# Performance work log

Measured on AMD Instinct MI355X. Metric: run time of the kernel, lower is better.

The kernel has to match this reference:

```python
import jax, jax.numpy as jnp
import numpy as np

B, S, D, H, DFF = 2, 2048, 1024, 16, 4096
DH = D // H
EPS = 1e-12


def _layer_norm(x, g, b):
    mu = jnp.mean(x, axis=-1, keepdims=True)
    var = jnp.mean(jnp.square(x - mu), axis=-1, keepdims=True)
    return (x - mu) * jax.lax.rsqrt(var + EPS) * g + b


def setup_inputs() -> dict:
    key = jax.random.key(0)
    ks = jax.random.split(key, 12)
    s = 0.02
    return {
        "query": jax.random.normal(ks[0], (B, S, D), jnp.float32),
        "key_in": jax.random.normal(ks[1], (B, S, D), jnp.float32),
        "value_in": jax.random.normal(ks[2], (B, S, D), jnp.float32),
        "attention_mask": jnp.zeros((B, 1, 1, S), jnp.float32),
        # weights stored [in, out] (i.e., torch Linear weight transposed)
        "Wq": jax.random.normal(ks[3], (D, D), jnp.float32) * s,
        "bq": jnp.zeros((D,), jnp.float32),
        "Wk": jax.random.normal(ks[4], (D, D), jnp.float32) * s,
        "bk": jnp.zeros((D,), jnp.float32),
        "Wv": jax.random.normal(ks[5], (D, D), jnp.float32) * s,
        "bv": jnp.zeros((D,), jnp.float32),
        "Wo": jax.random.normal(ks[6], (D, D), jnp.float32) * s,
        "bo": jnp.zeros((D,), jnp.float32),
        "ln1_g": jnp.ones((D,), jnp.float32),
        "ln1_b": jnp.zeros((D,), jnp.float32),
        "Wi": jax.random.normal(ks[7], (D, DFF), jnp.float32) * s,
        "bi": jnp.zeros((DFF,), jnp.float32),
        "Wd": jax.random.normal(ks[8], (DFF, D), jnp.float32) * s,
        "bd": jnp.zeros((D,), jnp.float32),
        "ln2_g": jnp.ones((D,), jnp.float32),
        "ln2_b": jnp.zeros((D,), jnp.float32),
    }


def reference(query, key_in, value_in, attention_mask, Wq, bq, Wk, bk, Wv, bv,
              Wo, bo, ln1_g, ln1_b, Wi, bi, Wd, bd, ln2_g, ln2_b):
    # projections -> [B, H, S, DH]
    q = (query @ Wq + bq).reshape(B, S, H, DH).transpose(0, 2, 1, 3)
    k = (key_in @ Wk + bk).reshape(B, S, H, DH).transpose(0, 2, 1, 3)
    v = (value_in @ Wv + bv).reshape(B, S, H, DH).transpose(0, 2, 1, 3)
    # eager attention: full [B,H,S,S] score matrix, as in the source
    scores = jnp.einsum("bhqd,bhkd->bhqk", q, k) / jnp.sqrt(jnp.float32(DH))
    scores = scores + attention_mask
    probs = jax.nn.softmax(scores, axis=-1)  # dropout p=0 -> identity
    ctx = jnp.einsum("bhqk,bhkd->bhqd", probs, v)
    ctx = ctx.transpose(0, 2, 1, 3).reshape(B, S, D)
    attn_out = ctx @ Wo + bo
    attn_out = _layer_norm(attn_out + query, ln1_g, ln1_b)
    inter = jax.nn.gelu(attn_out @ Wi + bi, approximate=False)
    layer_out = inter @ Wd + bd
    return _layer_norm(layer_out + attn_out, ln2_g, ln2_b)
```

## Files before the change

### kernel.cpp

```cpp
#include <hip/hip_runtime.h>
#include <hip/hip_bf16.h>
#include <cmath>

#define B_   2
#define S_   2048
#define D_   1024
#define H_   16
#define DFF_ 4096
#define DH_  64
#define M_   (B_*S_)

typedef __bf16 bfx8 __attribute__((ext_vector_type(8)));
typedef __bf16 bfx4 __attribute__((ext_vector_type(4)));
typedef float  fx4  __attribute__((ext_vector_type(4)));

__device__ __forceinline__ float fast_exp2(float x) {
  float r;
  asm volatile("v_exp_f32 %0, %1" : "=v"(r) : "v"(x));
  return r;
}

__device__ __forceinline__ float fast_erf(float x) {
  float ax = fabsf(x);
  float t  = __builtin_amdgcn_rcpf(fmaf(0.3275911f, ax, 1.0f));
  float p  = fmaf(1.061405429f, t, -1.453152027f);
  p = fmaf(p, t, 1.421413741f);
  p = fmaf(p, t, -0.284496736f);
  p = fmaf(p, t, 0.254829592f);
  p = p * t;
  float e  = fast_exp2(-ax * ax * 1.44269504f);
  float r  = 1.0f - p * e;
  return copysignf(r, x);
}

__device__ __forceinline__ void gload_lds16(const void* g, void* l) {
  __builtin_amdgcn_global_load_lds((__attribute__((address_space(1))) void*)(g),
                                   (__attribute__((address_space(3))) void*)(l),
                                   16, 0, 0);
}

struct CvtArgs { const float* in[3]; __bf16* out[3]; };

__global__ __launch_bounds__(256)
void to_bf16_3_kernel(CvtArgs args, int n) {
  int z = blockIdx.y;
  int i = (blockIdx.x * 256 + threadIdx.x) * 4;
  if (i < n) {
    float4 v = *(const float4*)(args.in[z] + i);
    bfx4 o;
    o[0] = (__bf16)v.x; o[1] = (__bf16)v.y; o[2] = (__bf16)v.z; o[3] = (__bf16)v.w;
    *(bfx4*)(args.out[z] + i) = o;
  }
}

__global__ __launch_bounds__(256)
void scale_mask_kernel(const float* __restrict__ in, float* __restrict__ out, int n) {
  int i = blockIdx.x * 256 + threadIdx.x;
  if (i < n) out[i] = in[i] * 1.44269504f;
}

__global__ __launch_bounds__(256)
void transpose_conv_kernel(const float* __restrict__ in, __bf16* __restrict__ out,
                           int R, int C) {
  __shared__ float t[32][33];
  int r0 = blockIdx.y * 32, c0 = blockIdx.x * 32;
  int tx = threadIdx.x, ty = threadIdx.y;
#pragma unroll
  for (int j = 0; j < 4; ++j) {
    int r = ty + j * 8;
    t[r][tx] = in[(size_t)(r0 + r) * C + c0 + tx];
  }
  __syncthreads();
#pragma unroll
  for (int j = 0; j < 4; ++j) {
    int c = ty + j * 8;
    out[(size_t)(c0 + c) * R + r0 + tx] = (__bf16)t[tx][c];
  }
}

__global__ __launch_bounds__(256)
void transpose_v_kernel(const __bf16* __restrict__ vb, __bf16* __restrict__ vt) {
  __shared__ __bf16 t[32][33];
  int bh = blockIdx.z;
  int b = bh >> 4, h = bh & 15;
  int s0 = blockIdx.x * 32, d0 = blockIdx.y * 32;
  int tx = threadIdx.x, ty = threadIdx.y;
#pragma unroll
  for (int j = 0; j < 4; ++j) {
    int s = ty + j * 8;
    t[s][tx] = vb[(size_t)((b * S_ + s0 + s) * H_ + h) * DH_ + d0 + tx];
  }
  __syncthreads();
#pragma unroll
  for (int j = 0; j < 4; ++j) {
    int d = ty + j * 8;
    vt[(size_t)(bh * DH_ + d0 + d) * S_ + s0 + tx] = t[tx][d];
  }
}

template<int MODE, int TBN>
__device__ __forceinline__ void gemm_body(const __bf16* __restrict__ A,
                                          const __bf16* __restrict__ Bt,
                                          const float* __restrict__ bias,
                                          const void* __restrict__ res,
                                          void* __restrict__ out,
                                          int Ndim, int Kdim,
                                          int m0, int n0,
                                          __bf16* As, __bf16* Bs) {
  const int tid  = threadIdx.x;
  const int lane = tid & 63;
  const int w    = tid >> 6;
  const int wm   = w >> 1, wn = w & 1;
  constexpr int NF = TBN / 32;

  fx4 acc[4][NF];
#pragma unroll
  for (int i = 0; i < 4; ++i)
#pragma unroll
    for (int j = 0; j < NF; ++j) acc[i][j] = {0.f, 0.f, 0.f, 0.f};

  const int KT = Kdim / 64;
  for (int kt = 0; kt < KT; ++kt) {
    __syncthreads();
    const int kb0 = kt * 64;
#pragma unroll
    for (int i = 0; i < 4; ++i) {
      int o   = tid * 16 + i * 4096;
      int row = o >> 7, cb = o & 127;
      int cbs = cb ^ ((row & 7) << 4);
      gload_lds16((const char*)A + ((size_t)(m0 + row) * Kdim + kb0) * 2 + cbs,
                  (char*)As + o);
    }
#pragma unroll
    for (int i = 0; i < TBN / 32; ++i) {
      int o   = tid * 16 + i * 4096;
      int row = o >> 7, cb = o & 127;
      int cbs = cb ^ ((row & 7) << 4);
      gload_lds16((const char*)Bt + ((size_t)(n0 + row) * Kdim + kb0) * 2 + cbs,
                  (char*)Bs + o);
    }
    __syncthreads();

#pragma unroll
    for (int kk = 0; kk < 2; ++kk) {
      bfx8 afr[4], bfr[NF];
      const int cb = kk * 64 + ((lane >> 4) << 4);
#pragma unroll
      for (int mf = 0; mf < 4; ++mf) {
        int row = wm * 64 + mf * 16 + (lane & 15);
        afr[mf] = *(const bfx8*)((const char*)As + row * 128 + (cb ^ ((row & 7) << 4)));
      }
#pragma unroll
      for (int nf = 0; nf < NF; ++nf) {
        int row = wn * (TBN / 2) + nf * 16 + (lane & 15);
        bfr[nf] = *(const bfx8*)((const char*)Bs + row * 128 + (cb ^ ((row & 7) << 4)));
      }
#pragma unroll
      for (int mf = 0; mf < 4; ++mf)
#pragma unroll
        for (int nf = 0; nf < NF; ++nf)
          acc[mf][nf] = __builtin_amdgcn_mfma_f32_16x16x32_bf16(afr[mf], bfr[nf],
                                                                acc[mf][nf], 0, 0, 0);
    }
  }

#pragma unroll
  for (int mf = 0; mf < 4; ++mf) {
#pragma unroll
    for (int nf = 0; nf < NF; ++nf) {
      int col = n0 + wn * (TBN / 2) + nf * 16 + (lane & 15);
      float bvl = bias[col];
#pragma unroll
      for (int r = 0; r < 4; ++r) {
        int rowg = m0 + wm * 64 + mf * 16 + ((lane >> 4) << 2) + r;
        float v = acc[mf][nf][r] + bvl;
        if (MODE == 2) v = 0.5f * v * (1.0f + fast_erf(v * 0.70710678118654752f));
        if (MODE == 4) v += (float)((const __bf16*)res)[(size_t)rowg * Ndim + col];
        if (MODE == 1) ((float*)out)[(size_t)rowg * Ndim + col] = v;
        else           ((__bf16*)out)[(size_t)rowg * Ndim + col] = (__bf16)v;
      }
    }
  }
}

template<int MODE, int TBN>
__global__ __launch_bounds__(256)
void gemm_kernel(const __bf16* __restrict__ A, const __bf16* __restrict__ Bt,
                 const float* __restrict__ bias, const void* __restrict__ res,
                 void* __restrict__ out, int Ndim, int Kdim) {
  __shared__ alignas(16) __bf16 As[128 * 64];
  __shared__ alignas(16) __bf16 Bs[TBN * 64];
  gemm_body<MODE, TBN>(A, Bt, bias, res, out, Ndim, Kdim,
                       blockIdx.y * 128, blockIdx.x * TBN, As, Bs);
}

__device__ __forceinline__ void stage_a256(const __bf16* __restrict__ A, int m0,
                                           int Kdim, int tile, int h, char* Asm) {
  char* dst = Asm + (tile & 1) * 32768;
  const int kb0 = tile * 64;
  const int tid = threadIdx.x;
#pragma unroll
  for (int it = 0; it < 2; ++it) {
    int o = tid * 16 + it * 8192;
    int lrow = o >> 7, cb = o & 127;
    int r = (lrow & 63) + h * 64 + ((lrow >> 6) << 7);
    int csrc = cb ^ ((r & 7) << 4);
    gload_lds16((const char*)A + ((size_t)(m0 + r) * Kdim + kb0) * 2 + csrc,
                dst + r * 128 + cb);
  }
}
__device__ __forceinline__ void stage_b256(const __bf16* __restrict__ Bt, int n0,
                                           int Kdim, int tile, int h, char* Bsm) {
  char* dst = Bsm + (tile & 1) * 32768;
  const int kb0 = tile * 64;
  const int tid = threadIdx.x;
#pragma unroll
  for (int it = 0; it < 2; ++it) {
    int o = tid * 16 + it * 8192;
    int lrow = o >> 7, cb = o & 127;
    int r = h * 128 + lrow;
    int csrc = cb ^ ((r & 7) << 4);
    gload_lds16((const char*)Bt + ((size_t)(n0 + r) * Kdim + kb0) * 2 + csrc,
                dst + r * 128 + cb);
  }
}

template<int MODE>
__device__ __forceinline__ void gemm256_body(const __bf16* __restrict__ A,
                                             const __bf16* __restrict__ Bt,
                                             const float* __restrict__ bias,
                                             void* __restrict__ out,
                                             int Ndim, int Kdim, int m0, int n0) {
  extern __shared__ char smem[];
  char* Asm = smem;
  char* Bsm = smem + 65536;
  const int tid  = threadIdx.x;
  const int lane = tid & 63;
  const int w    = tid >> 6;
  const int wm   = w >> 2;
  const int wn   = w & 3;
  const int g    = lane >> 4;
  const int ql   = lane & 15;
  const int KT   = Kdim / 64;

  fx4 acc[8][4];
#pragma unroll
  for (int i = 0; i < 8; ++i)
#pragma unroll
    for (int j = 0; j < 4; ++j) acc[i][j] = {0.f, 0.f, 0.f, 0.f};

  stage_a256(A, m0, Kdim, 0, 0, Asm);
  stage_a256(A, m0, Kdim, 0, 1, Asm);
  stage_b256(Bt, n0, Kdim, 0, 0, Bsm);
  stage_b256(Bt, n0, Kdim, 0, 1, Bsm);
  stage_a256(A, m0, Kdim, 1, 0, Asm);
  asm volatile("s_waitcnt vmcnt(2)" ::: "memory");
  __builtin_amdgcn_s_barrier();
  __builtin_amdgcn_sched_barrier(0);

  for (int t = 0; t < KT; ++t) {
    const char* Ab = Asm + (t & 1) * 32768;
    const char* Bb = Bsm + (t & 1) * 32768;
#pragma unroll
    for (int p = 0; p < 4; ++p) {
      const int ah = p >> 1, kk = p & 1;
      if (p == 0 && t + 1 < KT) stage_a256(A, m0, Kdim, t + 1, 1, Asm);
      if (p == 1 && t + 1 < KT) stage_b256(Bt, n0, Kdim, t + 1, 0, Bsm);
      if (p == 2 && t + 1 < KT) stage_b256(Bt, n0, Kdim, t + 1, 1, Bsm);
      if (p == 3 && t + 2 < KT) stage_a256(A, m0, Kdim, t + 2, 0, Asm);
      __builtin_amdgcn_sched_barrier(0);

      bfx8 af[4], bf[4];
      const int cbv = kk * 64 + g * 16;
#pragma unroll
      for (int j = 0; j < 4; ++j) {
        int arow = wm * 128 + (ah * 4 + j) * 16 + ql;
        af[j] = *(const bfx8*)(Ab + arow * 128 + (cbv ^ ((arow & 7) << 4)));
      }
#pragma unroll
      for (int nf = 0; nf < 4; ++nf) {
        int brow = wn * 64 + nf * 16 + ql;
        bf[nf] = *(const bfx8*)(Bb + brow * 128 + (cbv ^ ((brow & 7) << 4)));
      }
      __builtin_amdgcn_sched_barrier(0);
      __builtin_amdgcn_s_barrier();
      asm volatile("s_waitcnt lgkmcnt(0)" ::: "memory");
      __builtin_amdgcn_sched_barrier(0);
      __builtin_amdgcn_s_setprio(1);
#pragma unroll
      for (int j = 0; j < 4; ++j)
#pragma unroll
        for (int nf = 0; nf < 4; ++nf)
          acc[ah * 4 + j][nf] = __builtin_amdgcn_mfma_f32_16x16x32_bf16(
              af[j], bf[nf], acc[ah * 4 + j][nf], 0, 0, 0);
      __builtin_amdgcn_s_setprio(0);
      __builtin_amdgcn_s_barrier();
      __builtin_amdgcn_sched_barrier(0);
    }
    if (t + 1 < KT) {
      if (t + 2 < KT) asm volatile("s_waitcnt vmcnt(2)" ::: "memory");
      else            asm volatile("s_waitcnt vmcnt(0)" ::: "memory");
      __builtin_amdgcn_s_barrier();
      __builtin_amdgcn_sched_barrier(0);
    }
  }

#pragma unroll
  for (int mf = 0; mf < 8; ++mf) {
#pragma unroll
    for (int nf = 0; nf < 4; ++nf) {
      int col = n0 + wn * 64 + nf * 16 + ql;
      float bvl = bias[col];
#pragma unroll
      for (int r = 0; r < 4; ++r) {
        int rowg = m0 + wm * 128 + mf * 16 + g * 4 + r;
        float v = acc[mf][nf][r] + bvl;
        if (MODE == 2) v = 0.5f * v * (1.0f + fast_erf(v * 0.70710678118654752f));
        if (MODE == 1) ((float*)out)[(size_t)rowg * Ndim + col] = v;
        else          ((__bf16*)out)[(size_t)rowg * Ndim + col] = (__bf16)v;
      }
    }
  }
}

template<int MODE>
__global__ __launch_bounds__(512)
void gemm256_kernel(const __bf16* __restrict__ A, const __bf16* __restrict__ Bt,
                    const float* __restrict__ bias, void* __restrict__ out,
                    int Ndim, int Kdim) {
  gemm256_body<MODE>(A, Bt, bias, out, Ndim, Kdim,
                     blockIdx.y * 256, blockIdx.x * 256);
}

struct QKVArgs {
  const __bf16* A[3]; const __bf16* Bt[3]; const float* bias[3]; __bf16* out[3];
};

__global__ __launch_bounds__(512)
void qkv256_kernel(QKVArgs args, int Ndim, int Kdim) {
  int z = blockIdx.z;
  gemm256_body<0>(args.A[z], args.Bt[z], args.bias[z], (void*)args.out[z],
                  Ndim, Kdim, blockIdx.y * 256, blockIdx.x * 256);
}

__global__ __launch_bounds__(512)
void attn_kernel(const __bf16* __restrict__ Qb, const __bf16* __restrict__ Kb,
                 const __bf16* __restrict__ Vt, const float* __restrict__ mask2,
                 __bf16* __restrict__ ctx) {
  __shared__ alignas(16) __bf16 Ks[3 * 64 * 64];
  __shared__ alignas(16) __bf16 Vs[3 * 64 * 64];
  __shared__ alignas(16) __bf16 Ps[8 * 16 * 64];
  __shared__ alignas(16) float  Ms[2048];

  const int tid  = threadIdx.x;
  const int lane = tid & 63;
  const int w    = tid >> 6;
  const int g    = lane >> 4;
  const int ql   = lane & 15;
  const int bh   = blockIdx.y;
  const int b    = bh >> 4;
  const int h    = bh & 15;
  const int q0   = blockIdx.x * 128;

  const size_t kbase  = ((size_t)(b * S_)) * D_ + h * DH_;
  const size_t vtbase = (size_t)bh * DH_ * S_;
  const int NT = S_ / 64;

  char* Qsm = (char*)Ps;
  const size_t qbase = ((size_t)(b * S_) + q0) * D_ + h * DH_;
#pragma unroll
  for (int i = 0; i < 2; ++i) {
    int o   = tid * 16 + i * 8192;
    int row = o >> 7, cb = o & 127;
    int cbs = cb ^ ((row & 7) << 4);
    gload_lds16((const char*)Qb + (qbase + (size_t)row * D_) * 2 + cbs, Qsm + o);
  }
  {
    int o = tid * 16;
    gload_lds16((const char*)mask2 + (size_t)b * S_ * 4 + o, (char*)Ms + o);
  }
  {
    int o   = tid * 16;
    int row = o >> 7, cb = o & 127;
    int cbs = cb ^ ((row & 7) << 4);
    gload_lds16((const char*)Kb + (kbase + (size_t)row * D_) * 2 + cbs, (char*)Ks + o);
    gload_lds16((const char*)Vt + (vtbase + (size_t)row * S_) * 2 + cbs, (char*)Vs + o);
    gload_lds16((const char*)Kb + (kbase + (size_t)(64 + row) * D_) * 2 + cbs,
                (char*)Ks + 8192 + o);
    gload_lds16((const char*)Vt + (vtbase + (size_t)row * S_ + 64) * 2 + cbs,
                (char*)Vs + 8192 + o);
  }
  asm volatile("s_waitcnt vmcnt(4)" ::: "memory");
  __builtin_amdgcn_s_barrier();
  __builtin_amdgcn_sched_barrier(0);

  bfx8 aq[2];
  {
    int row = w * 16 + ql;
#pragma unroll
    for (int kk = 0; kk < 2; ++kk) {
      int cb = kk * 64 + g * 16;
      aq[kk] = *(const bfx8*)(Qsm + row * 128 + (cb ^ ((row & 7) << 4)));
    }
  }
  __syncthreads();
  asm volatile("s_waitcnt vmcnt(2)" ::: "memory");
  __builtin_amdgcn_s_barrier();
  __builtin_amdgcn_sched_barrier(0);

  float mrun = -1e30f, lrun = 0.f;
  fx4 acc[4];
#pragma unroll
  for (int d = 0; d < 4; ++d) acc[d] = {0.f, 0.f, 0.f, 0.f};

  char* pw = (char*)Ps + w * 2048;
  const float SCL = 0.18033688f;

  for (int t = 0; t < NT; ++t) {
    const int kv0 = t * 64;
    if (t + 2 < NT) {
      int o   = tid * 16;
      int row = o >> 7, cb = o & 127;
      int cbs = cb ^ ((row & 7) << 4);
      int nkv = kv0 + 128;
      int bo  = ((t + 2) % 3) * 8192;
      gload_lds16((const char*)Kb + (kbase + (size_t)(nkv + row) * D_) * 2 + cbs,
                  (char*)Ks + bo + o);
      gload_lds16((const char*)Vt + (vtbase + (size_t)row * S_ + nkv) * 2 + cbs,
                  (char*)Vs + bo + o);
    }
    __builtin_amdgcn_sched_barrier(0);
    if (t > 0) {
      if (t + 2 < NT)      asm volatile("s_waitcnt vmcnt(4)" ::: "memory");
      else if (t + 1 < NT) asm volatile("s_waitcnt vmcnt(2)" ::: "memory");
      else                 asm volatile("s_waitcnt vmcnt(0)" ::: "memory");
      __builtin_amdgcn_s_barrier();
      __builtin_amdgcn_sched_barrier(0);
    }
    const char* Kc = (const char*)Ks + (t % 3) * 8192;
    const char* Vc = (const char*)Vs + (t % 3) * 8192;

    fx4 sc[4];
#pragma unroll
    for (int nf = 0; nf < 4; ++nf) sc[nf] = {0.f, 0.f, 0.f, 0.f};
#pragma unroll
    for (int kk = 0; kk < 2; ++kk) {
      const int cb = kk * 64 + g * 16;
      bfx8 bk[4];
#pragma unroll
      for (int nf = 0; nf < 4; ++nf) {
        int row = nf * 16 + ql;
        bk[nf] = *(const bfx8*)(Kc + row * 128 + (cb ^ ((row & 7) << 4)));
      }
#pragma unroll
      for (int nf = 0; nf < 4; ++nf)
        sc[nf] = __builtin_amdgcn_mfma_f32_16x16x32_bf16(bk[nf], aq[kk], sc[nf], 0, 0, 0);
    }

    float sv[4][4];
#pragma unroll
    for (int nf = 0; nf < 4; ++nf) {
      float4 mk = *(const float4*)((const char*)Ms + (kv0 + nf * 16 + g * 4) * 4);
      sv[nf][0] = sc[nf][0] * SCL + mk.x;
      sv[nf][1] = sc[nf][1] * SCL + mk.y;
      sv[nf][2] = sc[nf][2] * SCL + mk.z;
      sv[nf][3] = sc[nf][3] * SCL + mk.w;
    }
    float t0 = fmaxf(fmaxf(sv[0][0], sv[0][1]), fmaxf(sv[0][2], sv[0][3]));
    float t1 = fmaxf(fmaxf(sv[1][0], sv[1][1]), fmaxf(sv[1][2], sv[1][3]));
    float t2 = fmaxf(fmaxf(sv[2][0], sv[2][1]), fmaxf(sv[2][2], sv[2][3]));
    float t3 = fmaxf(fmaxf(sv[3][0], sv[3][1]), fmaxf(sv[3][2], sv[3][3]));
    float mx = fmaxf(fmaxf(t0, t1), fmaxf(t2, t3));
    mx = fmaxf(mx, __shfl_xor(mx, 16));
    mx = fmaxf(mx, __shfl_xor(mx, 32));

    if (!__all(mx <= mrun + 8.0f)) {
      float mnew  = fmaxf(mrun, mx);
      float alpha = fast_exp2(mrun - mnew);
      lrun *= alpha;
      float af[4];
#pragma unroll
      for (int r = 0; r < 4; ++r) af[r] = __shfl(alpha, g * 4 + r);
#pragma unroll
      for (int d = 0; d < 4; ++d)
#pragma unroll
        for (int r = 0; r < 4; ++r) acc[d][r] *= af[r];
      mrun = mnew;
    }

    float ps[4];
#pragma unroll
    for (int nf = 0; nf < 4; ++nf) {
#pragma unroll
      for (int r = 0; r < 4; ++r) sv[nf][r] = fast_exp2(sv[nf][r] - mrun);
      ps[nf] = (sv[nf][0] + sv[nf][1]) + (sv[nf][2] + sv[nf][3]);
    }
    float rs = (ps[0] + ps[1]) + (ps[2] + ps[3]);
    rs += __shfl_xor(rs, 16);
    rs += __shfl_xor(rs, 32);
    lrun += rs;

#pragma unroll
    for (int nf = 0; nf < 4; ++nf) {
      bfx4 pv;
      pv[0] = (__bf16)sv[nf][0]; pv[1] = (__bf16)sv[nf][1];
      pv[2] = (__bf16)sv[nf][2]; pv[3] = (__bf16)sv[nf][3];
      int c = (nf * 32 + g * 8) ^ ((ql & 7) << 4);
      *(bfx4*)(pw + ql * 128 + c) = pv;
    }

    asm volatile("s_waitcnt lgkmcnt(0)" ::: "memory");
    __builtin_amdgcn_sched_barrier(0);

#pragma unroll
    for (int kk = 0; kk < 2; ++kk) {
      int prow = ql;
      int cb   = kk * 64 + g * 16;
      bfx8 ap  = *(const bfx8*)((const char*)pw + prow * 128 + (cb ^ ((prow & 7) << 4)));
#pragma unroll
      for (int d = 0; d < 4; ++d) {
        int vrow = d * 16 + ql;
        bfx8 bv  = *(const bfx8*)(Vc + vrow * 128 + (cb ^ ((vrow & 7) << 4)));
        acc[d] = __builtin_amdgcn_mfma_f32_16x16x32_bf16(ap, bv, acc[d], 0, 0, 0);
      }
    }

    __builtin_amdgcn_s_barrier();
    __builtin_amdgcn_sched_barrier(0);
  }

  float linv = 1.0f / lrun;
#pragma unroll
  for (int r = 0; r < 4; ++r) {
    float inv = __shfl(linv, g * 4 + r);
    int qrow = q0 + w * 16 + g * 4 + r;
    size_t base = ((size_t)(b * S_) + qrow) * D_ + h * DH_;
#pragma unroll
    for (int d = 0; d < 4; ++d)
      ctx[base + d * 16 + ql] = (__bf16)(acc[d][r] * inv);
  }
}

template<bool WRITE_BF16>
__global__ __launch_bounds__(256)
void ln_kernel(const __bf16* __restrict__ a,
               const float* __restrict__ g, const float* __restrict__ beta,
               float* __restrict__ outf, __bf16* __restrict__ outb) {
  const int row = blockIdx.x;
  const int tid = threadIdx.x;
  const size_t base = (size_t)row * D_;
  bfx4 xa = *(const bfx4*)(a + base + tid * 4);
  float x[4] = {(float)xa[0], (float)xa[1], (float)xa[2], (float)xa[3]};
  float s = x[0] + x[1] + x[2] + x[3];
#pragma unroll
  for (int m = 1; m < 64; m <<= 1) s += __shfl_xor(s, m);
  __shared__ float red[8];
  if ((tid & 63) == 0) red[tid >> 6] = s;
  __syncthreads();
  float mu = (red[0] + red[1] + red[2] + red[3]) * (1.0f / D_);
  float v0 = 0.f;
#pragma unroll
  for (int i = 0; i < 4; ++i) { float d = x[i] - mu; v0 += d * d; }
#pragma unroll
  for (int m = 1; m < 64; m <<= 1) v0 += __shfl_xor(v0, m);
  if ((tid & 63) == 0) red[4 + (tid >> 6)] = v0;
  __syncthreads();
  float var = (red[4] + red[5] + red[6] + red[7]) * (1.0f / D_);
  float rs = rsqrtf(var + 1e-12f);
#pragma unroll
  for (int i = 0; i < 4; ++i) {
    int col = tid * 4 + i;
    x[i] = (x[i] - mu) * rs * g[col] + beta[col];
  }
  if (WRITE_BF16) {
    bfx4 o;
    o[0] = (__bf16)x[0]; o[1] = (__bf16)x[1]; o[2] = (__bf16)x[2]; o[3] = (__bf16)x[3];
    *(bfx4*)(outb + base + tid * 4) = o;
  } else {
    *(float4*)(outf + base + tid * 4) = make_float4(x[0], x[1], x[2], x[3]);
  }
}

extern "C" void kernel_launch(void* const* d_in, const int* in_sizes, int n_in,
                              void* d_out, int out_size, void* d_ws, size_t ws_size,
                              hipStream_t stream) {
  const float* query    = (const float*)d_in[0];
  const float* key_in   = (const float*)d_in[1];
  const float* value_in = (const float*)d_in[2];
  const float* mask     = (const float*)d_in[3];
  const float* Wq = (const float*)d_in[4];  const float* bq = (const float*)d_in[5];
  const float* Wk = (const float*)d_in[6];  const float* bk = (const float*)d_in[7];
  const float* Wv = (const float*)d_in[8];  const float* bv = (const float*)d_in[9];
  const float* Wo = (const float*)d_in[10]; const float* bo = (const float*)d_in[11];
  const float* ln1g = (const float*)d_in[12]; const float* ln1b = (const float*)d_in[13];
  const float* Wi = (const float*)d_in[14]; const float* bi = (const float*)d_in[15];
  const float* Wd = (const float*)d_in[16]; const float* bd = (const float*)d_in[17];
  const float* ln2g = (const float*)d_in[18]; const float* ln2b = (const float*)d_in[19];

  char* ws = (char*)d_ws;
  const size_t MB = 1ull << 20;
  if (ws_size < 112 * MB) return;

  __bf16* xq   = (__bf16*)(ws + 0 * MB);
  __bf16* xk   = (__bf16*)(ws + 8 * MB);
  float*  mask2= (float*)(ws + 8 * MB);
  __bf16* xv   = (__bf16*)(ws + 16 * MB);
  __bf16* x1b  = (__bf16*)(ws + 16 * MB);
  __bf16* qb   = (__bf16*)(ws + 24 * MB);
  __bf16* inter= (__bf16*)(ws + 24 * MB);
  __bf16* kb   = (__bf16*)(ws + 32 * MB);
  __bf16* vb   = (__bf16*)(ws + 40 * MB);
  __bf16* alinb= (__bf16*)(ws + 40 * MB);
  __bf16* vt   = (__bf16*)(ws + 48 * MB);
  __bf16* ctxb = (__bf16*)(ws + 56 * MB);
  __bf16* ffb  = (__bf16*)(ws + 56 * MB);
  __bf16* wqt  = (__bf16*)(ws + 88 * MB);
  __bf16* wkt  = (__bf16*)(ws + 90 * MB);
  __bf16* wvt  = (__bf16*)(ws + 92 * MB);
  __bf16* wot  = (__bf16*)(ws + 94 * MB);
  __bf16* wit  = (__bf16*)(ws + 96 * MB);
  __bf16* wdt  = (__bf16*)(ws + 104 * MB);

  dim3 b256(256);
  dim3 tblk(32, 8);
  const int n1 = M_ * D_;

  CvtArgs ca;
  ca.in[0] = query; ca.in[1] = key_in; ca.in[2] = value_in;
  ca.out[0] = xq;   ca.out[1] = xk;    ca.out[2] = xv;
  to_bf16_3_kernel<<<dim3(n1 / 1024, 3), b256, 0, stream>>>(ca, n1);

  transpose_conv_kernel<<<dim3(D_ / 32, D_ / 32), tblk, 0, stream>>>(Wq, wqt, D_, D_);
  transpose_conv_kernel<<<dim3(D_ / 32, D_ / 32), tblk, 0, stream>>>(Wk, wkt, D_, D_);
  transpose_conv_kernel<<<dim3(D_ / 32, D_ / 32), tblk, 0, stream>>>(Wv, wvt, D_, D_);
  transpose_conv_kernel<<<dim3(D_ / 32, D_ / 32), tblk, 0, stream>>>(Wo, wot, D_, D_);
  transpose_conv_kernel<<<dim3(DFF_ / 32, D_ / 32), tblk, 0, stream>>>(Wi, wit, D_, DFF_);
  transpose_conv_kernel<<<dim3(D_ / 32, DFF_ / 32), tblk, 0, stream>>>(Wd, wdt, DFF_, D_);

  QKVArgs qa;
  qa.A[0] = xq;  qa.A[1] = xk;  qa.A[2] = xv;
  qa.Bt[0] = wqt; qa.Bt[1] = wkt; qa.Bt[2] = wvt;
  qa.bias[0] = bq; qa.bias[1] = bk; qa.bias[2] = bv;
  qa.out[0] = qb; qa.out[1] = kb; qa.out[2] = vb;
  qkv256_kernel<<<dim3(D_ / 256, M_ / 256, 3), dim3(512), 131072, stream>>>(qa, D_, D_);

  transpose_v_kernel<<<dim3(S_ / 32, 2, B_ * H_), tblk, 0, stream>>>(vb, vt);

  scale_mask_kernel<<<dim3((B_ * S_ + 255) / 256), b256, 0, stream>>>(mask, mask2, B_ * S_);

  attn_kernel<<<dim3(S_ / 128, B_ * H_), dim3(512), 0, stream>>>(qb, kb, vt, mask2, ctxb);

  gemm_kernel<4, 64><<<dim3(D_ / 64, M_ / 128), b256, 0, stream>>>(ctxb, wot, bo, xq, (void*)alinb, D_, D_);

  ln_kernel<true><<<dim3(M_), b256, 0, stream>>>(alinb, ln1g, ln1b, nullptr, x1b);

  gemm256_kernel<2><<<dim3(DFF_ / 256, M_ / 256), dim3(512), 131072, stream>>>(x1b, wit, bi, (void*)inter, DFF_, D_);

  gemm_kernel<4, 64><<<dim3(D_ / 64, M_ / 128), b256, 0, stream>>>(inter, wdt, bd, x1b, (void*)ffb, D_, DFF_);

  ln_kernel<false><<<dim3(M_), b256, 0, stream>>>(ffb, ln2g, ln2b, (float*)d_out, nullptr);
}
```

Before: 269.4 us.

## Double-buffer LDS in generic GEMM and batch weight transposes into one launch

```diff
diff --git a/kernel.cpp b/kernel.cpp
--- a/kernel.cpp
+++ b/kernel.cpp
@@ -59,12 +59,27 @@
   if (i < n) out[i] = in[i] * 1.44269504f;
 }
 
+struct TrArgs { const float* in[6]; __bf16* out[6]; };
+
 __global__ __launch_bounds__(256)
-void transpose_conv_kernel(const float* __restrict__ in, __bf16* __restrict__ out,
-                           int R, int C) {
+void transpose_all_kernel(TrArgs a) {
   __shared__ float t[32][33];
-  int r0 = blockIdx.y * 32, c0 = blockIdx.x * 32;
-  int tx = threadIdx.x, ty = threadIdx.y;
+  int bid = blockIdx.x;
+  int wsel, tr, tc, R, C;
+  if (bid < 4096) {
+    wsel = bid >> 10; int l = bid & 1023;
+    tr = l >> 5; tc = l & 31; R = D_; C = D_;
+  } else if (bid < 8192) {
+    wsel = 4; int l = bid - 4096;
+    tr = l >> 7; tc = l & 127; R = D_; C = DFF_;
+  } else {
+    wsel = 5; int l = bid - 8192;
+    tr = l >> 5; tc = l & 31; R = DFF_; C = D_;
+  }
+  const float* in = a.in[wsel];
+  __bf16* out = a.out[wsel];
+  int r0 = tr * 32, c0 = tc * 32;
+  int tx = threadIdx.x & 31, ty = threadIdx.x >> 5;
 #pragma unroll
   for (int j = 0; j < 4; ++j) {
     int r = ty + j * 8;
@@ -99,19 +114,18 @@
 }
 
 template<int MODE, int TBN>
-__device__ __forceinline__ void gemm_body(const __bf16* __restrict__ A,
-                                          const __bf16* __restrict__ Bt,
-                                          const float* __restrict__ bias,
-                                          const void* __restrict__ res,
-                                          void* __restrict__ out,
-                                          int Ndim, int Kdim,
-                                          int m0, int n0,
-                                          __bf16* As, __bf16* Bs) {
+__global__ __launch_bounds__(256)
+void gemm_kernel(const __bf16* __restrict__ A, const __bf16* __restrict__ Bt,
+                 const float* __restrict__ bias, const void* __restrict__ res,
+                 void* __restrict__ out, int Ndim, int Kdim) {
+  __shared__ alignas(16) __bf16 As[2 * 128 * 64];
+  __shared__ alignas(16) __bf16 Bs[2 * TBN * 64];
   const int tid  = threadIdx.x;
   const int lane = tid & 63;
   const int w    = tid >> 6;
   const int wm   = w >> 1, wn = w & 1;
   constexpr int NF = TBN / 32;
+  const int m0 = blockIdx.y * 128, n0 = blockIdx.x * TBN;
 
   fx4 acc[4][NF];
 #pragma unroll
@@ -120,8 +134,8 @@
     for (int j = 0; j < NF; ++j) acc[i][j] = {0.f, 0.f, 0.f, 0.f};
 
   const int KT = Kdim / 64;
-  for (int kt = 0; kt < KT; ++kt) {
-    __syncthreads();
+
+  auto stage = [&](int kt, int buf) {
     const int kb0 = kt * 64;
 #pragma unroll
     for (int i = 0; i < 4; ++i) {
@@ -129,17 +143,38 @@
       int row = o >> 7, cb = o & 127;
       int cbs = cb ^ ((row & 7) << 4);
       gload_lds16((const char*)A + ((size_t)(m0 + row) * Kdim + kb0) * 2 + cbs,
-                  (char*)As + o);
-    }
-#pragma unroll
-    for (int i = 0; i < TBN / 32; ++i) {
+                  (char*)As + buf * 16384 + o);
+    }
+#pragma unroll
+    for (int i = 0; i < NF; ++i) {
       int o   = tid * 16 + i * 4096;
       int row = o >> 7, cb = o & 127;
       int cbs = cb ^ ((row & 7) << 4);
       gload_lds16((const char*)Bt + ((size_t)(n0 + row) * Kdim + kb0) * 2 + cbs,
-                  (char*)Bs + o);
-    }
-    __syncthreads();
+                  (char*)Bs + buf * (TBN * 128) + o);
+    }
+  };
+
+  stage(0, 0);
+  asm volatile("s_waitcnt vmcnt(0)" ::: "memory");
+  __builtin_amdgcn_s_barrier();
+  __builtin_amdgcn_sched_barrier(0);
+
+  for (int kt = 0; kt < KT; ++kt) {
+    if (kt + 1 < KT) stage(kt + 1, (kt + 1) & 1);
+    __builtin_amdgcn_sched_barrier(0);
+    if (kt > 0) {
+      if (kt + 1 < KT) {
+        if constexpr (TBN == 64) asm volatile("s_waitcnt vmcnt(6)" ::: "memory");
+        else                     asm volatile("s_waitcnt vmcnt(8)" ::: "memory");
+      } else {
+        asm volatile("s_waitcnt vmcnt(0)" ::: "memory");
+      }
+      __builtin_amdgcn_s_barrier();
+      __builtin_amdgcn_sched_barrier(0);
+    }
+    const char* Ab = (const char*)As + (kt & 1) * 16384;
+    const char* Bb = (const char*)Bs + (kt & 1) * (TBN * 128);
 
 #pragma unroll
     for (int kk = 0; kk < 2; ++kk) {
@@ -148,12 +183,12 @@
 #pragma unroll
       for (int mf = 0; mf < 4; ++mf) {
         int row = wm * 64 + mf * 16 + (lane & 15);
-        afr[mf] = *(const bfx8*)((const char*)As + row * 128 + (cb ^ ((row & 7) << 4)));
+        afr[mf] = *(const bfx8*)(Ab + row * 128 + (cb ^ ((row & 7) << 4)));
       }
 #pragma unroll
       for (int nf = 0; nf < NF; ++nf) {
         int row = wn * (TBN / 2) + nf * 16 + (lane & 15);
-        bfr[nf] = *(const bfx8*)((const char*)Bs + row * 128 + (cb ^ ((row & 7) << 4)));
+        bfr[nf] = *(const bfx8*)(Bb + row * 128 + (cb ^ ((row & 7) << 4)));
       }
 #pragma unroll
       for (int mf = 0; mf < 4; ++mf)
@@ -162,6 +197,8 @@
           acc[mf][nf] = __builtin_amdgcn_mfma_f32_16x16x32_bf16(afr[mf], bfr[nf],
                                                                 acc[mf][nf], 0, 0, 0);
     }
+    __builtin_amdgcn_s_barrier();
+    __builtin_amdgcn_sched_barrier(0);
   }
 
 #pragma unroll
@@ -181,17 +218,6 @@
       }
     }
   }
-}
-
-template<int MODE, int TBN>
-__global__ __launch_bounds__(256)
-void gemm_kernel(const __bf16* __restrict__ A, const __bf16* __restrict__ Bt,
-                 const float* __restrict__ bias, const void* __restrict__ res,
-                 void* __restrict__ out, int Ndim, int Kdim) {
-  __shared__ alignas(16) __bf16 As[128 * 64];
-  __shared__ alignas(16) __bf16 Bs[TBN * 64];
-  gemm_body<MODE, TBN>(A, Bt, bias, res, out, Ndim, Kdim,
-                       blockIdx.y * 128, blockIdx.x * TBN, As, Bs);
 }
 
 __device__ __forceinline__ void stage_a256(const __bf16* __restrict__ A, int m0,
@@ -630,12 +656,11 @@
   ca.out[0] = xq;   ca.out[1] = xk;    ca.out[2] = xv;
   to_bf16_3_kernel<<<dim3(n1 / 1024, 3), b256, 0, stream>>>(ca, n1);
 
-  transpose_conv_kernel<<<dim3(D_ / 32, D_ / 32), tblk, 0, stream>>>(Wq, wqt, D_, D_);
-  transpose_conv_kernel<<<dim3(D_ / 32, D_ / 32), tblk, 0, stream>>>(Wk, wkt, D_, D_);
-  transpose_conv_kernel<<<dim3(D_ / 32, D_ / 32), tblk, 0, stream>>>(Wv, wvt, D_, D_);
-  transpose_conv_kernel<<<dim3(D_ / 32, D_ / 32), tblk, 0, stream>>>(Wo, wot, D_, D_);
-  transpose_conv_kernel<<<dim3(DFF_ / 32, D_ / 32), tblk, 0, stream>>>(Wi, wit, D_, DFF_);
-  transpose_conv_kernel<<<dim3(D_ / 32, DFF_ / 32), tblk, 0, stream>>>(Wd, wdt, DFF_, D_);
+  TrArgs ta;
+  ta.in[0] = Wq; ta.in[1] = Wk; ta.in[2] = Wv; ta.in[3] = Wo; ta.in[4] = Wi; ta.in[5] = Wd;
+  ta.out[0] = wqt; ta.out[1] = wkt; ta.out[2] = wvt; ta.out[3] = wot;
+  ta.out[4] = wit; ta.out[5] = wdt;
+  transpose_all_kernel<<<dim3(12288), b256, 0, stream>>>(ta);
 
   QKVArgs qa;
   qa.A[0] = xq;  qa.A[1] = xk;  qa.A[2] = xv;
```

New measurement: 257.3 us. 1.05x faster.
